# Performance work log

Hardware: AMD Instinct MI355X
Metric: run time of the kernel (lower is better)

Reference implementation:

```python
import jax, jax.numpy as jnp
import numpy as np

NUM_HEADS = 8
LN_EPS = 1e-5


def layernorm(x, w, b):
    mu = jnp.mean(x, axis=-1, keepdims=True)
    var = jnp.mean(jnp.square(x - mu), axis=-1, keepdims=True)
    return (x - mu) * jax.lax.rsqrt(var + LN_EPS) * w + b


def setup_inputs() -> dict:
    key = jax.random.key(0)
    ks = jax.random.split(key, 10)
    b, L, dim, hw = 16, 100, 512, 128 * 128
    s = 0.02
    return {
        "query": jax.random.normal(ks[0], (b, L, dim), jnp.float32),
        "feats": jax.random.normal(ks[1], (b, hw, dim), jnp.float32),
        "Wq": jax.random.normal(ks[2], (dim, dim), jnp.float32) * s,
        "Wk": jax.random.normal(ks[3], (dim, dim), jnp.float32) * s,
        "Wv": jax.random.normal(ks[4], (dim, dim), jnp.float32) * s,
        "Wp": jax.random.normal(ks[5], (dim, dim), jnp.float32) * s,
        "bp": jnp.zeros((dim,), jnp.float32),
        "W1": jax.random.normal(ks[6], (dim, dim), jnp.float32) * s,
        "b1": jnp.zeros((dim,), jnp.float32),
        "W2": jax.random.normal(ks[7], (dim, dim), jnp.float32) * s,
        "b2": jnp.zeros((dim,), jnp.float32),
        "ln0_w": jnp.ones((dim,), jnp.float32),
        "ln0_b": jnp.zeros((dim,), jnp.float32),
        "ln2_w": jnp.ones((dim,), jnp.float32),
        "ln2_b": jnp.zeros((dim,), jnp.float32),
    }


def reference(query, feats, Wq, Wk, Wv, Wp, bp, W1, b1, W2, b2, ln0_w, ln0_b, ln2_w, ln2_b):
    b, L, dim = query.shape
    hw = feats.shape[1]
    h = w = int(np.sqrt(hw))
    H = NUM_HEADS
    hd = dim // H
    scale = hd ** (-0.5)

    # torch nn.Linear: y = x @ W.T (no bias for q,k,v)
    q = (query @ Wq.T).reshape(b, L, H, hd) * scale
    k = (feats @ Wk.T).reshape(b, hw, H, hd)
    v = (feats @ Wv.T).reshape(b, hw, H, hd)

    # raw pre-softmax scores kept for the auxiliary mask output
    attn = jnp.einsum('blhd,bmhd->bhlm', q, k)        # [b, H, L, hw]
    attn_n = jax.nn.softmax(attn, axis=-1)
    out = jnp.einsum('bhlm,bmhd->blhd', attn_n, v).reshape(b, L, dim)

    x = layernorm(query + out @ Wp.T + bp, ln0_w, ln0_b)

    # FFN (dropouts are identity in eval)
    ffn = jax.nn.relu(x @ W1.T + b1) @ W2.T + b2
    y = layernorm(x + ffn, ln2_w, ln2_b)

    mask = attn.sum(axis=1).reshape(b, L, h, w)        # sum raw scores over heads
    return y, mask
```

## Files before the change

kernel.cpp:

```cpp
#include <hip/hip_runtime.h>
#include <hip/hip_bf16.h>
#include <math.h>

#define B_ 16
#define L_ 100
#define D_ 512
#define HW_ 16384
#define H_ 8

using bf16x8 = __attribute__((ext_vector_type(8))) short;
using f32x4  = __attribute__((ext_vector_type(4))) float;

__device__ __forceinline__ unsigned short f2bf(float x) {
    unsigned u = __float_as_uint(x);
    u += 0x7fffu + ((u >> 16) & 1u);
    return (unsigned short)(u >> 16);
}
__device__ __forceinline__ float bf2f(unsigned short b) {
    return __uint_as_float(((unsigned)b) << 16);
}

__global__ __launch_bounds__(256) void gemm_bt(
    const float* __restrict__ A, const float* __restrict__ Bm,
    const float* __restrict__ Cres, const float* __restrict__ bias,
    float* __restrict__ C,
    int M, int N, int K, int lda, int ldb, int ldc,
    int zmod, long sA, long sB, long sC1, long sC2,
    float alpha, int relu)
{
    const int z = blockIdx.z;
    const long aOff = (long)z * sA;
    const long bOff = (long)(z % zmod) * sB;
    const long cOff = (long)(z / zmod) * sC1 + (long)(z % zmod) * sC2;

    __shared__ float As[16][65];
    __shared__ float Bs[16][65];

    const int tid = threadIdx.x;
    const int tx = tid & 15, ty = tid >> 4;
    const int m0 = blockIdx.y * 64, n0 = blockIdx.x * 64;
    const int lr = tid & 63;
    const int lk = (tid >> 6) * 4;

    float acc[4][4];
#pragma unroll
    for (int i = 0; i < 4; ++i)
#pragma unroll
        for (int j = 0; j < 4; ++j) acc[i][j] = 0.f;

    for (int k0 = 0; k0 < K; k0 += 16) {
        __syncthreads();
        {
            float4 v = make_float4(0.f, 0.f, 0.f, 0.f);
            const int gr = m0 + lr;
            if (gr < M) v = *(const float4*)&A[aOff + (long)gr * lda + k0 + lk];
            As[lk + 0][lr] = v.x; As[lk + 1][lr] = v.y;
            As[lk + 2][lr] = v.z; As[lk + 3][lr] = v.w;
            const float4 w = *(const float4*)&Bm[bOff + (long)(n0 + lr) * ldb + k0 + lk];
            Bs[lk + 0][lr] = w.x; Bs[lk + 1][lr] = w.y;
            Bs[lk + 2][lr] = w.z; Bs[lk + 3][lr] = w.w;
        }
        __syncthreads();
#pragma unroll
        for (int k = 0; k < 16; ++k) {
            float a[4], bb[4];
#pragma unroll
            for (int i = 0; i < 4; ++i) a[i] = As[k][ty + 16 * i];
#pragma unroll
            for (int j = 0; j < 4; ++j) bb[j] = Bs[k][tx + 16 * j];
#pragma unroll
            for (int i = 0; i < 4; ++i)
#pragma unroll
                for (int j = 0; j < 4; ++j) acc[i][j] += a[i] * bb[j];
        }
    }

#pragma unroll
    for (int i = 0; i < 4; ++i) {
        const int r = m0 + ty + 16 * i;
        if (r >= M) continue;
#pragma unroll
        for (int j = 0; j < 4; ++j) {
            const int c = n0 + tx + 16 * j;
            float vv = alpha * acc[i][j];
            if (bias) vv += bias[c];
            if (Cres) vv += Cres[cOff + (long)r * ldc + c];
            if (relu) vv = fmaxf(vv, 0.f);
            C[cOff + (long)r * ldc + c] = vv;
        }
    }
}

__global__ __launch_bounds__(256) void qw_kernel(
    const float* __restrict__ q, const float* __restrict__ Wk,
    float* __restrict__ qw)
{
    const int bz = blockIdx.x;
    const int b = bz >> 3, h = bz & 7;
    __shared__ float q_s[L_][64];

    const int tid = threadIdx.x;
#pragma unroll
    for (int t = 0; t < 25; ++t) {
        const int idx = tid + 256 * t;
        const int l = idx >> 6, d = idx & 63;
        q_s[l][d] = q[((long)(b * L_ + l)) * D_ + h * 64 + d];
    }
    __syncthreads();

    const float* Wh = Wk + (long)h * 64 * D_;
    for (int lb = 0; lb < 10; ++lb) {
        float acc0[10], acc1[10];
#pragma unroll
        for (int ll = 0; ll < 10; ++ll) { acc0[ll] = 0.f; acc1[ll] = 0.f; }
        for (int d = 0; d < 64; ++d) {
            const float w0 = Wh[(long)d * D_ + tid];
            const float w1 = Wh[(long)d * D_ + tid + 256];
#pragma unroll
            for (int ll = 0; ll < 10; ++ll) {
                const float qv = q_s[lb * 10 + ll][d];
                acc0[ll] += qv * w0;
                acc1[ll] += qv * w1;
            }
        }
#pragma unroll
        for (int ll = 0; ll < 10; ++ll) {
            const long o = (((long)(b * H_ + h)) * L_ + lb * 10 + ll) * D_;
            qw[o + tid] = acc0[ll];
            qw[o + tid + 256] = acc1[ll];
        }
    }
}

#define MT_ 128

__global__ __launch_bounds__(256, 2) void flash_attn(
    const float* __restrict__ qw, const float* __restrict__ feats,
    float* __restrict__ ctx, float* __restrict__ mask_out)
{
    __shared__ __align__(16) char smem[70400];
    unsigned short* const qwlo = (unsigned short*)smem;
    char* const reg1 = smem + 33280;
    unsigned short* const fh  = (unsigned short*)reg1;
    unsigned short* const fl  = fh + 9216;
    float*          const ssf = (float*)reg1;
    unsigned short* const phl = (unsigned short*)(reg1 + 16896);
    unsigned short* const pll = phl + 4352;
    unsigned short* const fth = (unsigned short*)reg1;
    unsigned short* const ftl = fth + 8704;
    float* const alpha_s = (float*)(smem + 70144);
    float* const sum_s   = alpha_s + 32;

    const int tid  = threadIdx.x;
    const int lane = tid & 63;
    const int w    = tid >> 6;
    const int mw   = w >> 1;
    const int nw   = w & 1;
    const int ln15 = lane & 15;
    const int kl8  = (lane >> 4) * 8;
    const int kl4  = (lane >> 4) * 4;

    const int blk = blockIdx.x;
    const int b   = blk / 25;
    const int l0  = (blk % 25) * 4;

    const f32x4 fzero = {0.f, 0.f, 0.f, 0.f};

    const int hl_a = mw * 16 + ln15;
    const int h_a = hl_a >> 2, li_a = hl_a & 3;
    const float* qrow = qw + (((long)(b * H_ + h_a)) * L_ + (l0 + li_a)) * D_;

    bf16x8 qhf[16];
#pragma unroll
    for (int kt = 0; kt < 16; ++kt) {
        float4 v0 = *(const float4*)&qrow[kt * 32 + kl8];
        float4 v1 = *(const float4*)&qrow[kt * 32 + kl8 + 4];
        float xs[8] = {v0.x, v0.y, v0.z, v0.w, v1.x, v1.y, v1.z, v1.w};
        bf16x8 qv;
        unsigned short ll[8];
#pragma unroll
        for (int e = 0; e < 8; ++e) {
            unsigned short hhv = f2bf(xs[e]);
            ll[e] = f2bf(xs[e] - bf2f(hhv));
            qv[e] = (short)hhv;
        }
        qhf[kt] = qv;
        if (nw == 0) {
            unsigned short* dst = &qwlo[hl_a * 520 + kt * 32 + kl8];
#pragma unroll
            for (int e = 0; e < 8; ++e) dst[e] = ll[e];
        }
    }

    float run_max = -INFINITY, run_sum = 0.f;
    const int srow = tid >> 3, slan = tid & 7;

    f32x4 cacc[8][2];
#pragma unroll
    for (int i = 0; i < 8; ++i)
#pragma unroll
        for (int j = 0; j < 2; ++j) cacc[i][j] = fzero;

    const long fbase = (long)b * HW_ * D_;

    for (int m0 = 0; m0 < HW_; m0 += MT_) {
        f32x4 sacc[4];
#pragma unroll
        for (int t = 0; t < 4; ++t) sacc[t] = fzero;

#pragma unroll
        for (int dc = 0; dc < 8; ++dc) {
            __syncthreads();
            {
                float4 vv[8];
#pragma unroll
                for (int it = 0; it < 8; ++it) {
                    int f4 = tid + 256 * it;
                    int r = f4 >> 4, c4 = f4 & 15;
                    vv[it] = *(const float4*)&feats[fbase + (long)(m0 + r) * D_ + dc * 64 + c4 * 4];
                }
#pragma unroll
                for (int it = 0; it < 8; ++it) {
                    int f4 = tid + 256 * it;
                    int r = f4 >> 4, c4 = f4 & 15;
                    float xs[4] = {vv[it].x, vv[it].y, vv[it].z, vv[it].w};
                    unsigned short hh[4], ll[4];
#pragma unroll
                    for (int e = 0; e < 4; ++e) {
                        hh[e] = f2bf(xs[e]);
                        ll[e] = f2bf(xs[e] - bf2f(hh[e]));
                    }
                    uint2 hp, lp;
                    hp.x = (unsigned)hh[0] | ((unsigned)hh[1] << 16);
                    hp.y = (unsigned)hh[2] | ((unsigned)hh[3] << 16);
                    lp.x = (unsigned)ll[0] | ((unsigned)ll[1] << 16);
                    lp.y = (unsigned)ll[2] | ((unsigned)ll[3] << 16);
                    *(uint2*)&fh[r * 72 + c4 * 4] = hp;
                    *(uint2*)&fl[r * 72 + c4 * 4] = lp;
                }
            }
            __syncthreads();
#pragma unroll
            for (int kt = 0; kt < 2; ++kt) {
                bf16x8 qlv = *(const bf16x8*)&qwlo[hl_a * 520 + dc * 64 + kt * 32 + kl8];
                bf16x8 qhv = qhf[dc * 2 + kt];
#pragma unroll
                for (int t = 0; t < 4; ++t) {
                    const int nt = nw + 2 * t;
                    const unsigned short* bp = &fh[(nt * 16 + ln15) * 72 + kt * 32 + kl8];
                    bf16x8 bhv = *(const bf16x8*)bp;
                    bf16x8 blv = *(const bf16x8*)(bp + 9216);
                    sacc[t] = __builtin_amdgcn_mfma_f32_16x16x32_bf16(qhv, bhv, sacc[t], 0, 0, 0);
                    sacc[t] = __builtin_amdgcn_mfma_f32_16x16x32_bf16(qhv, blv, sacc[t], 0, 0, 0);
                    sacc[t] = __builtin_amdgcn_mfma_f32_16x16x32_bf16(qlv, bhv, sacc[t], 0, 0, 0);
                }
            }
        }

        __syncthreads();
#pragma unroll
        for (int t = 0; t < 4; ++t) {
#pragma unroll
            for (int r = 0; r < 4; ++r)
                ssf[(mw * 16 + kl4 + r) * 132 + (nw + 2 * t) * 16 + ln15] = sacc[t][r];
        }
        __syncthreads();

        {
            const int li = tid >> 6, mm = tid & 63;
#pragma unroll
            for (int rep = 0; rep < 2; ++rep) {
                const int m = mm + 64 * rep;
                float s = 0.f;
#pragma unroll
                for (int hh2 = 0; hh2 < 8; ++hh2) s += ssf[(hh2 * 4 + li) * 132 + m];
                mask_out[((long)(b * L_ + l0 + li)) * HW_ + m0 + m] = s;
            }
        }

        {
            float v[16];
            float mx = -INFINITY;
#pragma unroll
            for (int k = 0; k < 16; ++k) {
                v[k] = ssf[srow * 132 + slan * 16 + k];
                mx = fmaxf(mx, v[k]);
            }
#pragma unroll
            for (int o = 4; o > 0; o >>= 1) mx = fmaxf(mx, __shfl_xor(mx, o, 8));
            const float nm = fmaxf(run_max, mx);
            const float al = __expf(run_max - nm);
            float cs = 0.f;
            unsigned hp[8], lp[8];
#pragma unroll
            for (int j = 0; j < 8; ++j) {
                float p0 = __expf(v[2 * j]     - nm);
                float p1 = __expf(v[2 * j + 1] - nm);
                cs += p0 + p1;
                unsigned short h0 = f2bf(p0), h1 = f2bf(p1);
                unsigned short q0 = f2bf(p0 - bf2f(h0)), q1 = f2bf(p1 - bf2f(h1));
                hp[j] = (unsigned)h0 | ((unsigned)h1 << 16);
                lp[j] = (unsigned)q0 | ((unsigned)q1 << 16);
            }
            *(uint4*)&phl[srow * 136 + slan * 16]     = make_uint4(hp[0], hp[1], hp[2], hp[3]);
            *(uint4*)&phl[srow * 136 + slan * 16 + 8] = make_uint4(hp[4], hp[5], hp[6], hp[7]);
            *(uint4*)&pll[srow * 136 + slan * 16]     = make_uint4(lp[0], lp[1], lp[2], lp[3]);
            *(uint4*)&pll[srow * 136 + slan * 16 + 8] = make_uint4(lp[4], lp[5], lp[6], lp[7]);
#pragma unroll
            for (int o = 4; o > 0; o >>= 1) cs += __shfl_xor(cs, o, 8);
            run_sum = run_sum * al + cs;
            run_max = nm;
            if (slan == 0) alpha_s[srow] = al;
        }
        __syncthreads();

        bf16x8 pha[4], pla[4];
#pragma unroll
        for (int kt = 0; kt < 4; ++kt) {
            pha[kt] = *(const bf16x8*)&phl[(mw * 16 + ln15) * 136 + kt * 32 + kl8];
            pla[kt] = *(const bf16x8*)&pll[(mw * 16 + ln15) * 136 + kt * 32 + kl8];
        }
        float alr[4];
#pragma unroll
        for (int r = 0; r < 4; ++r) alr[r] = alpha_s[mw * 16 + kl4 + r];
#pragma unroll
        for (int i = 0; i < 8; ++i)
#pragma unroll
            for (int j = 0; j < 2; ++j)
#pragma unroll
                for (int r = 0; r < 4; ++r) cacc[i][j][r] *= alr[r];

#pragma unroll
        for (int dc = 0; dc < 8; ++dc) {
            __syncthreads();
            {
                const int mq = tid & 15, dq = tid >> 4;
#pragma unroll
                for (int mh = 0; mh < 2; ++mh) {
                    float4 vv[4];
#pragma unroll
                    for (int i = 0; i < 4; ++i)
                        vv[i] = *(const float4*)&feats[fbase + (long)(m0 + mh * 64 + mq * 4 + i) * D_ + dc * 64 + dq * 4];
#pragma unroll
                    for (int j = 0; j < 4; ++j) {
                        unsigned short hh[4], ll[4];
#pragma unroll
                        for (int i = 0; i < 4; ++i) {
                            float x = ((const float*)&vv[i])[j];
                            hh[i] = f2bf(x);
                            ll[i] = f2bf(x - bf2f(hh[i]));
                        }
                        uint2 hp2, lp2;
                        hp2.x = (unsigned)hh[0] | ((unsigned)hh[1] << 16);
                        hp2.y = (unsigned)hh[2] | ((unsigned)hh[3] << 16);
                        lp2.x = (unsigned)ll[0] | ((unsigned)ll[1] << 16);
                        lp2.y = (unsigned)ll[2] | ((unsigned)ll[3] << 16);
                        *(uint2*)&fth[(dq * 4 + j) * 136 + mh * 64 + mq * 4] = hp2;
                        *(uint2*)&ftl[(dq * 4 + j) * 136 + mh * 64 + mq * 4] = lp2;
                    }
                }
            }
            __syncthreads();
#pragma unroll
            for (int kt = 0; kt < 4; ++kt) {
#pragma unroll
                for (int t = 0; t < 2; ++t) {
                    const int nt = nw + 2 * t;
                    const unsigned short* bp = &fth[(nt * 16 + ln15) * 136 + kt * 32 + kl8];
                    bf16x8 bhv = *(const bf16x8*)bp;
                    bf16x8 blv = *(const bf16x8*)(bp + 8704);
                    cacc[dc][t] = __builtin_amdgcn_mfma_f32_16x16x32_bf16(pha[kt], bhv, cacc[dc][t], 0, 0, 0);
                    cacc[dc][t] = __builtin_amdgcn_mfma_f32_16x16x32_bf16(pha[kt], blv, cacc[dc][t], 0, 0, 0);
                    cacc[dc][t] = __builtin_amdgcn_mfma_f32_16x16x32_bf16(pla[kt], bhv, cacc[dc][t], 0, 0, 0);
                }
            }
        }
    }

    if (slan == 0) sum_s[srow] = run_sum;
    __syncthreads();
#pragma unroll
    for (int r = 0; r < 4; ++r) {
        const int hl = mw * 16 + kl4 + r;
        const float inv = 1.f / sum_s[hl];
        const int h = hl >> 2, li = hl & 3;
        const long base = (((long)(b * H_ + h)) * L_ + (l0 + li)) * D_;
#pragma unroll
        for (int i = 0; i < 8; ++i)
#pragma unroll
            for (int j = 0; j < 2; ++j)
                ctx[base + i * 64 + (nw + 2 * j) * 16 + ln15] = cacc[i][j][r] * inv;
    }
}

__global__ __launch_bounds__(256) void ln_kernel(
    const float* __restrict__ X, const float* __restrict__ w,
    const float* __restrict__ bb, float* __restrict__ out)
{
    const int row = blockIdx.x;
    const int tid = threadIdx.x;
    const long base = (long)row * D_;
    const float x0 = X[base + tid];
    const float x1 = X[base + tid + 256];
    float s = x0 + x1;
    float sq = x0 * x0 + x1 * x1;
#pragma unroll
    for (int o = 32; o > 0; o >>= 1) {
        s  += __shfl_xor(s, o, 64);
        sq += __shfl_xor(sq, o, 64);
    }
    __shared__ float ws_[4], wq_[4];
    const int wid = tid >> 6, lane = tid & 63;
    if (lane == 0) { ws_[wid] = s; wq_[wid] = sq; }
    __syncthreads();
    s  = ws_[0] + ws_[1] + ws_[2] + ws_[3];
    sq = wq_[0] + wq_[1] + wq_[2] + wq_[3];
    const float mu = s * (1.f / 512.f);
    const float var = sq * (1.f / 512.f) - mu * mu;
    const float rs = rsqrtf(var + 1e-5f);
    out[base + tid]       = (x0 - mu) * rs * w[tid] + bb[tid];
    out[base + tid + 256] = (x1 - mu) * rs * w[tid + 256] + bb[tid + 256];
}

extern "C" void kernel_launch(void* const* d_in, const int* in_sizes, int n_in,
                              void* d_out, int out_size, void* d_ws, size_t ws_size,
                              hipStream_t stream)
{
    const float* query = (const float*)d_in[0];
    const float* feats = (const float*)d_in[1];
    const float* Wq    = (const float*)d_in[2];
    const float* Wk    = (const float*)d_in[3];
    const float* Wv    = (const float*)d_in[4];
    const float* Wp    = (const float*)d_in[5];
    const float* bp    = (const float*)d_in[6];
    const float* W1    = (const float*)d_in[7];
    const float* b1    = (const float*)d_in[8];
    const float* W2    = (const float*)d_in[9];
    const float* b2    = (const float*)d_in[10];
    const float* ln0w  = (const float*)d_in[11];
    const float* ln0b  = (const float*)d_in[12];
    const float* ln2w  = (const float*)d_in[13];
    const float* ln2b  = (const float*)d_in[14];

    float* out = (float*)d_out;
    float* ws  = (float*)d_ws;

    float* q     = ws;
    float* qw    = ws + 819200;
    float* ctx   = ws + 7372800;
    float* attno = ws;
    float* xin   = ws + 7372800;
    float* x     = xin + 819200;
    float* h1    = x + 819200;
    float* ffnp  = h1 + 819200;

    const dim3 thr(256);

    gemm_bt<<<dim3(8, 25, 1), thr, 0, stream>>>(
        query, Wq, nullptr, nullptr, q,
        1600, 512, 512, 512, 512, 512, 1, 0, 0, 0, 0, 0.125f, 0);

    qw_kernel<<<dim3(128), thr, 0, stream>>>(q, Wk, qw);

    flash_attn<<<dim3(400), thr, 0, stream>>>(qw, feats, ctx, out + 819200);

    gemm_bt<<<dim3(1, 2, 128), thr, 0, stream>>>(
        ctx, Wv, nullptr, nullptr, attno,
        100, 64, 512, 512, 512, 512, 8, 51200, 32768, 51200, 64, 1.f, 0);

    gemm_bt<<<dim3(8, 25, 1), thr, 0, stream>>>(
        attno, Wp, query, bp, xin,
        1600, 512, 512, 512, 512, 512, 1, 0, 0, 0, 0, 1.f, 0);

    ln_kernel<<<dim3(1600), thr, 0, stream>>>(xin, ln0w, ln0b, x);

    gemm_bt<<<dim3(8, 25, 1), thr, 0, stream>>>(
        x, W1, nullptr, b1, h1,
        1600, 512, 512, 512, 512, 512, 1, 0, 0, 0, 0, 1.f, 1);

    gemm_bt<<<dim3(8, 25, 1), thr, 0, stream>>>(
        h1, W2, x, b2, ffnp,
        1600, 512, 512, 512, 512, 512, 1, 0, 0, 0, 0, 1.f, 0);

    ln_kernel<<<dim3(1600), thr, 0, stream>>>(ffnp, ln2w, ln2b, out);
}
```

Baseline: 6.071 ms.

## Prefetch feats into registers, swizzle LDS, pre-split qw, raise occupancy

Reworks the flash attention kernel. The next feats chunk is now loaded into registers while MFMAs run on the current chunk, and the LDS tiles use an XOR-swizzled layout with no padding, which shrinks shared memory so launch bounds can allow 3 blocks per CU. The hi/lo bf16 split of qw moves into qw_kernel, and the split uses truncation and perm instead of round-to-nearest. The block-to-batch mapping is also reordered for L2 locality. In exchange, register pressure rises and the truncating split changes numerics slightly.

```diff
diff --git a/kernel.cpp b/kernel.cpp
--- a/kernel.cpp
+++ b/kernel.cpp
@@ -18,6 +18,17 @@
 }
 __device__ __forceinline__ float bf2f(unsigned short b) {
     return __uint_as_float(((unsigned)b) << 16);
+}
+__device__ __forceinline__ unsigned prm(unsigned hi, unsigned lo) {
+#if defined(__has_builtin)
+#if __has_builtin(__builtin_amdgcn_perm)
+    return __builtin_amdgcn_perm(hi, lo, 0x07060302u);
+#else
+    return (lo >> 16) | (hi & 0xFFFF0000u);
+#endif
+#else
+    return (lo >> 16) | (hi & 0xFFFF0000u);
+#endif
 }
 
 __global__ __launch_bounds__(256) void gemm_bt(
@@ -93,7 +104,7 @@
 
 __global__ __launch_bounds__(256) void qw_kernel(
     const float* __restrict__ q, const float* __restrict__ Wk,
-    float* __restrict__ qw)
+    unsigned short* __restrict__ qwh, unsigned short* __restrict__ qwl)
 {
     const int bz = blockIdx.x;
     const int b = bz >> 3, h = bz & 7;
@@ -126,143 +137,169 @@
 #pragma unroll
         for (int ll = 0; ll < 10; ++ll) {
             const long o = (((long)(b * H_ + h)) * L_ + lb * 10 + ll) * D_;
-            qw[o + tid] = acc0[ll];
-            qw[o + tid + 256] = acc1[ll];
-        }
-    }
-}
-
-#define MT_ 128
-
-__global__ __launch_bounds__(256, 2) void flash_attn(
-    const float* __restrict__ qw, const float* __restrict__ feats,
+            const unsigned short h0 = f2bf(acc0[ll]);
+            const unsigned short h1 = f2bf(acc1[ll]);
+            qwh[o + tid]       = h0;
+            qwh[o + tid + 256] = h1;
+            qwl[o + tid]       = f2bf(acc0[ll] - bf2f(h0));
+            qwl[o + tid + 256] = f2bf(acc1[ll] - bf2f(h1));
+        }
+    }
+}
+
+__global__ __launch_bounds__(256, 3) void flash_attn(
+    const unsigned short* __restrict__ qwh,
+    const unsigned short* __restrict__ qwl,
+    const float* __restrict__ feats,
     float* __restrict__ ctx, float* __restrict__ mask_out)
 {
-    __shared__ __align__(16) char smem[70400];
-    unsigned short* const qwlo = (unsigned short*)smem;
-    char* const reg1 = smem + 33280;
-    unsigned short* const fh  = (unsigned short*)reg1;
-    unsigned short* const fl  = fh + 9216;
-    float*          const ssf = (float*)reg1;
-    unsigned short* const phl = (unsigned short*)(reg1 + 16896);
-    unsigned short* const pll = phl + 4352;
-    unsigned short* const fth = (unsigned short*)reg1;
-    unsigned short* const ftl = fth + 8704;
-    float* const alpha_s = (float*)(smem + 70144);
-    float* const sum_s   = alpha_s + 32;
+    __shared__ __align__(16) char smem[49408];
+    char* const R0 = smem;
+    char* const R1 = smem + 32768;
+    float* const alpha_s = (float*)(smem + 49152);
+    float* const sum_s   = (float*)(smem + 49280);
 
     const int tid  = threadIdx.x;
     const int lane = tid & 63;
     const int w    = tid >> 6;
-    const int mw   = w >> 1;
-    const int nw   = w & 1;
+    const int mw   = w >> 1, nw = w & 1;
     const int ln15 = lane & 15;
-    const int kl8  = (lane >> 4) * 8;
-    const int kl4  = (lane >> 4) * 4;
-
-    const int blk = blockIdx.x;
-    const int b   = blk / 25;
-    const int l0  = (blk % 25) * 4;
-
-    const f32x4 fzero = {0.f, 0.f, 0.f, 0.f};
+    const int lg   = lane >> 4;
+    const int kl8  = lg * 8, kl4 = lg * 4;
+
+    const int hwb  = blockIdx.x;
+    const int slot = hwb >> 3;
+    const int b    = (hwb & 7) * 2 + (slot >= 25 ? 1 : 0);
+    const int l0   = (slot >= 25 ? slot - 25 : slot) * 4;
+
+    const long fbase = (long)b * HW_ * D_;
 
     const int hl_a = mw * 16 + ln15;
-    const int h_a = hl_a >> 2, li_a = hl_a & 3;
-    const float* qrow = qw + (((long)(b * H_ + h_a)) * L_ + (l0 + li_a)) * D_;
-
-    bf16x8 qhf[16];
-#pragma unroll
-    for (int kt = 0; kt < 16; ++kt) {
-        float4 v0 = *(const float4*)&qrow[kt * 32 + kl8];
-        float4 v1 = *(const float4*)&qrow[kt * 32 + kl8 + 4];
-        float xs[8] = {v0.x, v0.y, v0.z, v0.w, v1.x, v1.y, v1.z, v1.w};
-        bf16x8 qv;
-        unsigned short ll[8];
-#pragma unroll
-        for (int e = 0; e < 8; ++e) {
-            unsigned short hhv = f2bf(xs[e]);
-            ll[e] = f2bf(xs[e] - bf2f(hhv));
-            qv[e] = (short)hhv;
-        }
-        qhf[kt] = qv;
-        if (nw == 0) {
-            unsigned short* dst = &qwlo[hl_a * 520 + kt * 32 + kl8];
-#pragma unroll
-            for (int e = 0; e < 8; ++e) dst[e] = ll[e];
-        }
-    }
+    const long qoff = (((long)(b * H_ + (hl_a >> 2))) * L_ + (l0 + (hl_a & 3))) * D_;
+
+    int offA[2][4];
+#pragma unroll
+    for (int t = 0; t < 4; ++t) {
+        const int r = (nw + 2 * t) * 16 + ln15;
+#pragma unroll
+        for (int kt = 0; kt < 2; ++kt)
+            offA[kt][t] = r * 128 + (((kt * 4 + lg) ^ (r & 7)) << 4);
+    }
+    int offB[4][2];
+#pragma unroll
+    for (int t = 0; t < 2; ++t) {
+        const int r = (nw + 2 * t) * 16 + ln15;
+#pragma unroll
+        for (int kt = 0; kt < 4; ++kt)
+            offB[kt][t] = r * 256 + (((kt * 4 + lg) ^ (r & 7)) << 4);
+    }
+    int offP[4];
+    {
+        const int r = mw * 16 + ln15;
+#pragma unroll
+        for (int kt = 0; kt < 4; ++kt)
+            offP[kt] = r * 512 + (((kt * 4 + lg) ^ (r & 7)) << 4);
+    }
+
+    const int srow = tid >> 3, slan = tid & 7;
+    const int mp = tid & 63;
 
     float run_max = -INFINITY, run_sum = 0.f;
-    const int srow = tid >> 3, slan = tid & 7;
-
     f32x4 cacc[8][2];
 #pragma unroll
     for (int i = 0; i < 8; ++i)
 #pragma unroll
-        for (int j = 0; j < 2; ++j) cacc[i][j] = fzero;
-
-    const long fbase = (long)b * HW_ * D_;
-
-    for (int m0 = 0; m0 < HW_; m0 += MT_) {
+        for (int j = 0; j < 2; ++j) cacc[i][j] = (f32x4){0.f, 0.f, 0.f, 0.f};
+
+    for (int m0 = 0; m0 < HW_; m0 += 128) {
         f32x4 sacc[4];
 #pragma unroll
-        for (int t = 0; t < 4; ++t) sacc[t] = fzero;
+        for (int t = 0; t < 4; ++t) sacc[t] = (f32x4){0.f, 0.f, 0.f, 0.f};
+
+        float4 vA[8];
+        bf16x8 nqh0, nqh1, nql0, nql1;
+        {
+            const float* fp = feats + fbase + (long)m0 * D_;
+#pragma unroll
+            for (int it = 0; it < 8; ++it) {
+                const int f4 = tid + 256 * it;
+                vA[it] = *(const float4*)&fp[(long)(f4 >> 4) * D_ + (f4 & 15) * 4];
+            }
+            nqh0 = *(const bf16x8*)(qwh + qoff + kl8);
+            nqh1 = *(const bf16x8*)(qwh + qoff + 32 + kl8);
+            nql0 = *(const bf16x8*)(qwl + qoff + kl8);
+            nql1 = *(const bf16x8*)(qwl + qoff + 32 + kl8);
+        }
 
 #pragma unroll
         for (int dc = 0; dc < 8; ++dc) {
+            const bf16x8 qh0 = nqh0, qh1 = nqh1, ql0 = nql0, ql1 = nql1;
             __syncthreads();
-            {
-                float4 vv[8];
+#pragma unroll
+            for (int it = 0; it < 8; ++it) {
+                const int f4 = tid + 256 * it;
+                const int r = f4 >> 4, c4 = f4 & 15;
+                const float4 vv = vA[it];
+                const unsigned u0 = __float_as_uint(vv.x), u1 = __float_as_uint(vv.y);
+                const unsigned u2 = __float_as_uint(vv.z), u3 = __float_as_uint(vv.w);
+                const float e0 = vv.x - __uint_as_float(u0 & 0xFFFF0000u);
+                const float e1 = vv.y - __uint_as_float(u1 & 0xFFFF0000u);
+                const float e2 = vv.z - __uint_as_float(u2 & 0xFFFF0000u);
+                const float e3 = vv.w - __uint_as_float(u3 & 0xFFFF0000u);
+                const int off = r * 128 + ((((c4 >> 1) ^ (r & 7)) << 4)) + ((c4 & 1) << 3);
+                *(uint2*)(R0 + off) = make_uint2(prm(u1, u0), prm(u3, u2));
+                *(uint2*)(R0 + 16384 + off) =
+                    make_uint2(prm(__float_as_uint(e1), __float_as_uint(e0)),
+                               prm(__float_as_uint(e3), __float_as_uint(e2)));
+            }
+            __syncthreads();
+            if (dc < 7) {
+                const float* fp = feats + fbase + (long)m0 * D_ + (dc + 1) * 64;
 #pragma unroll
                 for (int it = 0; it < 8; ++it) {
-                    int f4 = tid + 256 * it;
-                    int r = f4 >> 4, c4 = f4 & 15;
-                    vv[it] = *(const float4*)&feats[fbase + (long)(m0 + r) * D_ + dc * 64 + c4 * 4];
+                    const int f4 = tid + 256 * it;
+                    vA[it] = *(const float4*)&fp[(long)(f4 >> 4) * D_ + (f4 & 15) * 4];
                 }
-#pragma unroll
-                for (int it = 0; it < 8; ++it) {
-                    int f4 = tid + 256 * it;
-                    int r = f4 >> 4, c4 = f4 & 15;
-                    float xs[4] = {vv[it].x, vv[it].y, vv[it].z, vv[it].w};
-                    unsigned short hh[4], ll[4];
-#pragma unroll
-                    for (int e = 0; e < 4; ++e) {
-                        hh[e] = f2bf(xs[e]);
-                        ll[e] = f2bf(xs[e] - bf2f(hh[e]));
-                    }
-                    uint2 hp, lp;
-                    hp.x = (unsigned)hh[0] | ((unsigned)hh[1] << 16);
-                    hp.y = (unsigned)hh[2] | ((unsigned)hh[3] << 16);
-                    lp.x = (unsigned)ll[0] | ((unsigned)ll[1] << 16);
-                    lp.y = (unsigned)ll[2] | ((unsigned)ll[3] << 16);
-                    *(uint2*)&fh[r * 72 + c4 * 4] = hp;
-                    *(uint2*)&fl[r * 72 + c4 * 4] = lp;
+                const long qo = qoff + (dc + 1) * 64 + kl8;
+                nqh0 = *(const bf16x8*)(qwh + qo);
+                nqh1 = *(const bf16x8*)(qwh + qo + 32);
+                nql0 = *(const bf16x8*)(qwl + qo);
+                nql1 = *(const bf16x8*)(qwl + qo + 32);
+            }
+#pragma unroll
+            for (int kt = 0; kt < 2; ++kt) {
+                const bf16x8 qh = kt ? qh1 : qh0;
+                const bf16x8 ql = kt ? ql1 : ql0;
+#pragma unroll
+                for (int t = 0; t < 4; ++t) {
+                    const char* bp = R0 + offA[kt][t];
+                    const bf16x8 bh = *(const bf16x8*)bp;
+                    const bf16x8 bl = *(const bf16x8*)(bp + 16384);
+                    sacc[t] = __builtin_amdgcn_mfma_f32_16x16x32_bf16(qh, bh, sacc[t], 0, 0, 0);
+                    sacc[t] = __builtin_amdgcn_mfma_f32_16x16x32_bf16(qh, bl, sacc[t], 0, 0, 0);
+                    sacc[t] = __builtin_amdgcn_mfma_f32_16x16x32_bf16(ql, bh, sacc[t], 0, 0, 0);
                 }
             }
-            __syncthreads();
-#pragma unroll
-            for (int kt = 0; kt < 2; ++kt) {
-                bf16x8 qlv = *(const bf16x8*)&qwlo[hl_a * 520 + dc * 64 + kt * 32 + kl8];
-                bf16x8 qhv = qhf[dc * 2 + kt];
-#pragma unroll
-                for (int t = 0; t < 4; ++t) {
-                    const int nt = nw + 2 * t;
-                    const unsigned short* bp = &fh[(nt * 16 + ln15) * 72 + kt * 32 + kl8];
-                    bf16x8 bhv = *(const bf16x8*)bp;
-                    bf16x8 blv = *(const bf16x8*)(bp + 9216);
-                    sacc[t] = __builtin_amdgcn_mfma_f32_16x16x32_bf16(qhv, bhv, sacc[t], 0, 0, 0);
-                    sacc[t] = __builtin_amdgcn_mfma_f32_16x16x32_bf16(qhv, blv, sacc[t], 0, 0, 0);
-                    sacc[t] = __builtin_amdgcn_mfma_f32_16x16x32_bf16(qlv, bhv, sacc[t], 0, 0, 0);
-                }
-            }
-        }
-
-        __syncthreads();
+        }
+
+        float4 vB[8];
+        {
+            const float* fp = feats + fbase + (long)m0 * D_ + w * 16;
+#pragma unroll
+            for (int i = 0; i < 4; ++i) {
+                vB[2 * i]     = *(const float4*)&fp[(long)(2 * mp) * D_ + 4 * i];
+                vB[2 * i + 1] = *(const float4*)&fp[(long)(2 * mp + 1) * D_ + 4 * i];
+            }
+        }
+
 #pragma unroll
         for (int t = 0; t < 4; ++t) {
-#pragma unroll
-            for (int r = 0; r < 4; ++r)
-                ssf[(mw * 16 + kl4 + r) * 132 + (nw + 2 * t) * 16 + ln15] = sacc[t][r];
+            const int col = (nw + 2 * t) * 16 + ln15;
+#pragma unroll
+            for (int r = 0; r < 4; ++r) {
+                const int row = mw * 16 + kl4 + r;
+                *(float*)(R1 + row * 512 + ((((col >> 2) ^ (row & 7)) << 4)) + ((col & 3) << 2)) = sacc[t][r];
+            }
         }
         __syncthreads();
 
@@ -273,19 +310,26 @@
                 const int m = mm + 64 * rep;
                 float s = 0.f;
 #pragma unroll
-                for (int hh2 = 0; hh2 < 8; ++hh2) s += ssf[(hh2 * 4 + li) * 132 + m];
+                for (int hh = 0; hh < 8; ++hh) {
+                    const int row = hh * 4 + li;
+                    s += *(const float*)(R1 + row * 512 + ((((m >> 2) ^ (row & 7)) << 4)) + ((m & 3) << 2));
+                }
                 mask_out[((long)(b * L_ + l0 + li)) * HW_ + m0 + m] = s;
             }
         }
+        float v[16];
+#pragma unroll
+        for (int q4 = 0; q4 < 4; ++q4) {
+            const float4 t4 = *(const float4*)(R1 + srow * 512 + ((((slan * 4 + q4) ^ (srow & 7)) << 4)));
+            v[q4 * 4 + 0] = t4.x; v[q4 * 4 + 1] = t4.y;
+            v[q4 * 4 + 2] = t4.z; v[q4 * 4 + 3] = t4.w;
+        }
+        __syncthreads();
 
         {
-            float v[16];
-            float mx = -INFINITY;
-#pragma unroll
-            for (int k = 0; k < 16; ++k) {
-                v[k] = ssf[srow * 132 + slan * 16 + k];
-                mx = fmaxf(mx, v[k]);
-            }
+            float mx = v[0];
+#pragma unroll
+            for (int k = 1; k < 16; ++k) mx = fmaxf(mx, v[k]);
 #pragma unroll
             for (int o = 4; o > 0; o >>= 1) mx = fmaxf(mx, __shfl_xor(mx, o, 8));
             const float nm = fmaxf(run_max, mx);
@@ -294,18 +338,22 @@
             unsigned hp[8], lp[8];
 #pragma unroll
             for (int j = 0; j < 8; ++j) {
-                float p0 = __expf(v[2 * j]     - nm);
-                float p1 = __expf(v[2 * j + 1] - nm);
+                const float p0 = __expf(v[2 * j] - nm);
+                const float p1 = __expf(v[2 * j + 1] - nm);
                 cs += p0 + p1;
-                unsigned short h0 = f2bf(p0), h1 = f2bf(p1);
-                unsigned short q0 = f2bf(p0 - bf2f(h0)), q1 = f2bf(p1 - bf2f(h1));
-                hp[j] = (unsigned)h0 | ((unsigned)h1 << 16);
-                lp[j] = (unsigned)q0 | ((unsigned)q1 << 16);
-            }
-            *(uint4*)&phl[srow * 136 + slan * 16]     = make_uint4(hp[0], hp[1], hp[2], hp[3]);
-            *(uint4*)&phl[srow * 136 + slan * 16 + 8] = make_uint4(hp[4], hp[5], hp[6], hp[7]);
-            *(uint4*)&pll[srow * 136 + slan * 16]     = make_uint4(lp[0], lp[1], lp[2], lp[3]);
-            *(uint4*)&pll[srow * 136 + slan * 16 + 8] = make_uint4(lp[4], lp[5], lp[6], lp[7]);
+                const unsigned a = __float_as_uint(p0), bu = __float_as_uint(p1);
+                hp[j] = prm(bu, a);
+                const float q0 = p0 - __uint_as_float(a & 0xFFFF0000u);
+                const float q1 = p1 - __uint_as_float(bu & 0xFFFF0000u);
+                lp[j] = prm(__float_as_uint(q1), __float_as_uint(q0));
+            }
+            char* prow = R1 + srow * 512;
+            const int g0 = ((slan * 2) ^ (srow & 7)) << 4;
+            const int g1 = ((slan * 2 + 1) ^ (srow & 7)) << 4;
+            *(uint4*)(prow + g0) = make_uint4(hp[0], hp[1], hp[2], hp[3]);
+            *(uint4*)(prow + g1) = make_uint4(hp[4], hp[5], hp[6], hp[7]);
+            *(uint4*)(prow + 256 + g0) = make_uint4(lp[0], lp[1], lp[2], lp[3]);
+            *(uint4*)(prow + 256 + g1) = make_uint4(lp[4], lp[5], lp[6], lp[7]);
 #pragma unroll
             for (int o = 4; o > 0; o >>= 1) cs += __shfl_xor(cs, o, 8);
             run_sum = run_sum * al + cs;
@@ -314,64 +362,59 @@
         }
         __syncthreads();
 
-        bf16x8 pha[4], pla[4];
-#pragma unroll
-        for (int kt = 0; kt < 4; ++kt) {
-            pha[kt] = *(const bf16x8*)&phl[(mw * 16 + ln15) * 136 + kt * 32 + kl8];
-            pla[kt] = *(const bf16x8*)&pll[(mw * 16 + ln15) * 136 + kt * 32 + kl8];
-        }
-        float alr[4];
-#pragma unroll
-        for (int r = 0; r < 4; ++r) alr[r] = alpha_s[mw * 16 + kl4 + r];
-#pragma unroll
-        for (int i = 0; i < 8; ++i)
-#pragma unroll
-            for (int j = 0; j < 2; ++j)
-#pragma unroll
-                for (int r = 0; r < 4; ++r) cacc[i][j][r] *= alr[r];
+        {
+            float alr[4];
+#pragma unroll
+            for (int r = 0; r < 4; ++r) alr[r] = alpha_s[mw * 16 + kl4 + r];
+#pragma unroll
+            for (int i = 0; i < 8; ++i)
+#pragma unroll
+                for (int j = 0; j < 2; ++j)
+#pragma unroll
+                    for (int r = 0; r < 4; ++r) cacc[i][j][r] *= alr[r];
+        }
 
 #pragma unroll
         for (int dc = 0; dc < 8; ++dc) {
             __syncthreads();
-            {
-                const int mq = tid & 15, dq = tid >> 4;
-#pragma unroll
-                for (int mh = 0; mh < 2; ++mh) {
-                    float4 vv[4];
-#pragma unroll
-                    for (int i = 0; i < 4; ++i)
-                        vv[i] = *(const float4*)&feats[fbase + (long)(m0 + mh * 64 + mq * 4 + i) * D_ + dc * 64 + dq * 4];
-#pragma unroll
-                    for (int j = 0; j < 4; ++j) {
-                        unsigned short hh[4], ll[4];
-#pragma unroll
-                        for (int i = 0; i < 4; ++i) {
-                            float x = ((const float*)&vv[i])[j];
-                            hh[i] = f2bf(x);
-                            ll[i] = f2bf(x - bf2f(hh[i]));
-                        }
-                        uint2 hp2, lp2;
-                        hp2.x = (unsigned)hh[0] | ((unsigned)hh[1] << 16);
-                        hp2.y = (unsigned)hh[2] | ((unsigned)hh[3] << 16);
-                        lp2.x = (unsigned)ll[0] | ((unsigned)ll[1] << 16);
-                        lp2.y = (unsigned)ll[2] | ((unsigned)ll[3] << 16);
-                        *(uint2*)&fth[(dq * 4 + j) * 136 + mh * 64 + mq * 4] = hp2;
-                        *(uint2*)&ftl[(dq * 4 + j) * 136 + mh * 64 + mq * 4] = lp2;
-                    }
+#pragma unroll
+            for (int i = 0; i < 4; ++i) {
+                const float4 va = vB[2 * i], vb = vB[2 * i + 1];
+                const float af[4] = {va.x, va.y, va.z, va.w};
+                const float bf[4] = {vb.x, vb.y, vb.z, vb.w};
+#pragma unroll
+                for (int j = 0; j < 4; ++j) {
+                    const int d = w * 16 + 4 * i + j;
+                    const unsigned ua = __float_as_uint(af[j]);
+                    const unsigned ub = __float_as_uint(bf[j]);
+                    const float ea = af[j] - __uint_as_float(ua & 0xFFFF0000u);
+                    const float eb = bf[j] - __uint_as_float(ub & 0xFFFF0000u);
+                    const int off = d * 256 + ((((mp >> 2) ^ (d & 7)) << 4)) + ((mp & 3) << 2);
+                    *(unsigned*)(R0 + off) = prm(ub, ua);
+                    *(unsigned*)(R0 + 16384 + off) = prm(__float_as_uint(eb), __float_as_uint(ea));
                 }
             }
             __syncthreads();
+            if (dc < 7) {
+                const float* fp = feats + fbase + (long)m0 * D_ + (dc + 1) * 64 + w * 16;
+#pragma unroll
+                for (int i = 0; i < 4; ++i) {
+                    vB[2 * i]     = *(const float4*)&fp[(long)(2 * mp) * D_ + 4 * i];
+                    vB[2 * i + 1] = *(const float4*)&fp[(long)(2 * mp + 1) * D_ + 4 * i];
+                }
+            }
 #pragma unroll
             for (int kt = 0; kt < 4; ++kt) {
+                const bf16x8 ph = *(const bf16x8*)(R1 + offP[kt]);
+                const bf16x8 pl = *(const bf16x8*)(R1 + offP[kt] + 256);
 #pragma unroll
                 for (int t = 0; t < 2; ++t) {
-                    const int nt = nw + 2 * t;
-                    const unsigned short* bp = &fth[(nt * 16 + ln15) * 136 + kt * 32 + kl8];
-                    bf16x8 bhv = *(const bf16x8*)bp;
-                    bf16x8 blv = *(const bf16x8*)(bp + 8704);
-                    cacc[dc][t] = __builtin_amdgcn_mfma_f32_16x16x32_bf16(pha[kt], bhv, cacc[dc][t], 0, 0, 0);
-                    cacc[dc][t] = __builtin_amdgcn_mfma_f32_16x16x32_bf16(pha[kt], blv, cacc[dc][t], 0, 0, 0);
-                    cacc[dc][t] = __builtin_amdgcn_mfma_f32_16x16x32_bf16(pla[kt], bhv, cacc[dc][t], 0, 0, 0);
+                    const char* bp = R0 + offB[kt][t];
+                    const bf16x8 bh = *(const bf16x8*)bp;
+                    const bf16x8 bl = *(const bf16x8*)(bp + 16384);
+                    cacc[dc][t] = __builtin_amdgcn_mfma_f32_16x16x32_bf16(ph, bh, cacc[dc][t], 0, 0, 0);
+                    cacc[dc][t] = __builtin_amdgcn_mfma_f32_16x16x32_bf16(ph, bl, cacc[dc][t], 0, 0, 0);
+                    cacc[dc][t] = __builtin_amdgcn_mfma_f32_16x16x32_bf16(pl, bh, cacc[dc][t], 0, 0, 0);
                 }
             }
         }
@@ -383,13 +426,12 @@
     for (int r = 0; r < 4; ++r) {
         const int hl = mw * 16 + kl4 + r;
         const float inv = 1.f / sum_s[hl];
-        const int h = hl >> 2, li = hl & 3;
-        const long base = (((long)(b * H_ + h)) * L_ + (l0 + li)) * D_;
-#pragma unroll
-        for (int i = 0; i < 8; ++i)
-#pragma unroll
-            for (int j = 0; j < 2; ++j)
-                ctx[base + i * 64 + (nw + 2 * j) * 16 + ln15] = cacc[i][j][r] * inv;
+        const long base = (((long)(b * H_ + (hl >> 2))) * L_ + (l0 + (hl & 3))) * D_;
+#pragma unroll
+        for (int dc = 0; dc < 8; ++dc)
+#pragma unroll
+            for (int t = 0; t < 2; ++t)
+                ctx[base + dc * 64 + (nw + 2 * t) * 16 + ln15] = cacc[dc][t][r] * inv;
     }
 }
 
@@ -445,14 +487,15 @@
     float* out = (float*)d_out;
     float* ws  = (float*)d_ws;
 
-    float* q     = ws;
-    float* qw    = ws + 819200;
+    float* q = ws;
+    unsigned short* qwh = (unsigned short*)(ws + 819200);
+    unsigned short* qwl = (unsigned short*)(ws + 4096000);
     float* ctx   = ws + 7372800;
     float* attno = ws;
-    float* xin   = ws + 7372800;
-    float* x     = xin + 819200;
-    float* h1    = x + 819200;
-    float* ffnp  = h1 + 819200;
+    float* xin   = ws + 819200;
+    float* x     = ws + 1638400;
+    float* h1    = ws + 2457600;
+    float* ffnp  = ws + 3276800;
 
     const dim3 thr(256);
 
@@ -460,9 +503,9 @@
         query, Wq, nullptr, nullptr, q,
         1600, 512, 512, 512, 512, 512, 1, 0, 0, 0, 0, 0.125f, 0);
 
-    qw_kernel<<<dim3(128), thr, 0, stream>>>(q, Wk, qw);
-
-    flash_attn<<<dim3(400), thr, 0, stream>>>(qw, feats, ctx, out + 819200);
+    qw_kernel<<<dim3(128), thr, 0, stream>>>(q, Wk, qwh, qwl);
+
+    flash_attn<<<dim3(400), thr, 0, stream>>>(qwh, qwl, feats, ctx, out + 819200);
 
     gemm_bt<<<dim3(1, 2, 128), thr, 0, stream>>>(
         ctx, Wv, nullptr, nullptr, attno,
```

After: 7.018 ms. 1.16x slower.
